# Kernel tuning notes

Hardware: AMD Instinct MI355X
Metric: run time of the kernel (lower is better)

Reference implementation:

```python
import jax, jax.numpy as jnp
import numpy as np

B, S, HID = 2, 2048, 4096
NH, NKV, HD = 32, 8, 128
SLIDING_WINDOW = 1024
ROPE_THETA = 10000.0


def setup_inputs() -> dict:
    key = jax.random.key(0)
    ks = jax.random.split(key, 6)
    hidden_states = jax.random.normal(ks[0], (B, S, HID), dtype=jnp.float32)
    attention_mask = jnp.ones((B, S), dtype=jnp.int32)
    position_ids = jnp.broadcast_to(jnp.arange(S, dtype=jnp.int32)[None, :], (B, S))
    sc = 1.0 / np.sqrt(HID)
    q_w = jax.random.normal(ks[1], (HID, NH * HD), dtype=jnp.float32) * sc
    k_w = jax.random.normal(ks[2], (HID, NKV * HD), dtype=jnp.float32) * sc
    v_w = jax.random.normal(ks[3], (HID, NKV * HD), dtype=jnp.float32) * sc
    o_w = jax.random.normal(ks[4], (NH * HD, HID), dtype=jnp.float32) * sc
    return {"hidden_states": hidden_states, "attention_mask": attention_mask,
            "position_ids": position_ids, "q_w": q_w, "k_w": k_w, "v_w": v_w, "o_w": o_w}


def _rotate_half(x):
    return jnp.concatenate((-x[..., x.shape[-1] // 2:], x[..., : x.shape[-1] // 2]), axis=-1)


def _rope_sincos(position_ids):
    # inv_freq over even dims of head_dim; emb = concat(freqs, freqs)
    inv_freq = 1.0 / ROPE_THETA ** (jnp.arange(0, HD, 2, dtype=jnp.float32) / HD)
    freqs = position_ids.astype(jnp.float32)[..., None] * inv_freq  # [B,S,HD/2]
    emb = jnp.concatenate((freqs, freqs), axis=-1)                  # [B,S,HD]
    # broadcast over heads axis: [B,S,1,HD]
    return jnp.sin(emb)[:, :, None, :], jnp.cos(emb)[:, :, None, :]


def reference(hidden_states, attention_mask, position_ids, q_w, k_w, v_w, o_w):
    b, q_len, _ = hidden_states.shape
    n_rep = NH // NKV

    q = (hidden_states @ q_w).reshape(b, q_len, NH, HD)
    k = (hidden_states @ k_w).reshape(b, q_len, NKV, HD)
    v = (hidden_states @ v_w).reshape(b, q_len, NKV, HD)

    sin_pos, cos_pos = _rope_sincos(position_ids)
    q = q * cos_pos + _rotate_half(q) * sin_pos
    k = k * cos_pos + _rotate_half(k) * sin_pos

    # GQA: repeat kv heads (repeat_interleave along head axis)
    k = jnp.repeat(k, n_rep, axis=2)  # [B,S,NH,HD]
    v = jnp.repeat(v, n_rep, axis=2)

    # sliding-window causal mask: j <= i and j >= i - sliding_window
    i = jnp.arange(q_len)[:, None]
    j = jnp.arange(q_len)[None, :]
    band = (j <= i) & (j >= i - SLIDING_WINDOW)           # [Q,K]
    mask = band[None, None] & (attention_mask[:, None, None, :] > 0)  # [B,1,Q,K]

    bias = jnp.where(mask, 0.0, jnp.finfo(jnp.float32).min)

    scale = 1.0 / jnp.sqrt(jnp.asarray(HD, dtype=jnp.float32))
    scores = jnp.einsum('bqhd,bkhd->bhqk', q, k) * scale + bias
    attn_weights = jax.nn.softmax(scores, axis=-1)
    attn_out = jnp.einsum('bhqk,bkhd->bqhd', attn_weights, v)
    attn_out = attn_out.reshape(b, q_len, HID)
    return attn_out @ o_w
```

## Files before the change

kernel.cpp:

```cpp
#include <hip/hip_runtime.h>
#include <stdint.h>
#include <stddef.h>

typedef __bf16 bf16x8 __attribute__((ext_vector_type(8)));
typedef short short8 __attribute__((ext_vector_type(8)));
typedef float floatx4 __attribute__((ext_vector_type(4)));
typedef float f32x16 __attribute__((ext_vector_type(16)));
typedef unsigned short ushort4v __attribute__((ext_vector_type(4)));
typedef unsigned int uint2v __attribute__((ext_vector_type(2)));

__device__ __forceinline__ unsigned short f2bf(float f){
  unsigned int u = __float_as_uint(f);
  u += 0x7fffu + ((u >> 16) & 1u);
  return (unsigned short)(u >> 16);
}
__device__ __forceinline__ float bf2f(unsigned short s){
  return __uint_as_float(((unsigned int)s) << 16);
}
__device__ __forceinline__ void gl2lds16(const void* g, void* l){
  __builtin_amdgcn_global_load_lds((const __attribute__((address_space(1))) void*)g,
                                   (__attribute__((address_space(3))) void*)l, 16, 0, 0);
}

__global__ __launch_bounds__(256) void conv_f32_bf16(const float* __restrict__ in,
                                                     unsigned short* __restrict__ out){
  int t = blockIdx.x * 256 + threadIdx.x;
  floatx4 v = *(const floatx4*)(in + (size_t)t * 4);
  ushort4v o;
#pragma unroll
  for (int j = 0; j < 4; ++j) o[j] = f2bf(v[j]);
  *(ushort4v*)(out + (size_t)t * 4) = o;
}

__global__ __launch_bounds__(256) void transpose_cvt(const float* __restrict__ in,
                                                     unsigned short* __restrict__ out,
                                                     int Kd, int Nd){
  __shared__ __align__(16) unsigned short tile[64 * 80];
  int n0 = blockIdx.x * 64, k0 = blockIdx.y * 64;
  int t = threadIdx.x;
#pragma unroll
  for (int it = 0; it < 2; ++it){
    int rr = (t >> 3) + it * 32;
    int cc = t & 7;
    const float* src = in + (size_t)(k0 + rr) * Nd + n0 + cc * 8;
    floatx4 a = *(const floatx4*)src;
    floatx4 b = *(const floatx4*)(src + 4);
    short8 s;
#pragma unroll
    for (int j = 0; j < 4; ++j){ s[j] = (short)f2bf(a[j]); s[j + 4] = (short)f2bf(b[j]); }
    *(short8*)&tile[rr * 80 + cc * 8] = s;
  }
  __syncthreads();
#pragma unroll
  for (int it = 0; it < 2; ++it){
    int nr = (t >> 3) + it * 32;
    int kc = t & 7;
    short8 v;
#pragma unroll
    for (int j = 0; j < 8; ++j) v[j] = (short)tile[(kc * 8 + j) * 80 + nr];
    *(short8*)(out + (size_t)(n0 + nr) * Kd + k0 + kc * 8) = v;
  }
}

__global__ __launch_bounds__(512, 2) void gemm_bt(
    const unsigned short* __restrict__ A,
    const unsigned short* __restrict__ Wq,
    const unsigned short* __restrict__ Wk,
    const unsigned short* __restrict__ Wv,
    unsigned short* __restrict__ oQ,
    unsigned short* __restrict__ oK,
    unsigned short* __restrict__ oVt,
    float* __restrict__ oF, int f32out)
{
  __shared__ __align__(16) unsigned short As[2][256 * 64];
  __shared__ __align__(16) unsigned short Bs[2][256 * 64];
  const int tid = threadIdx.x;
  const int w = tid >> 6, lane = tid & 63, quad = lane >> 4, l15 = lane & 15;
  const int wr = w >> 2, wc = w & 3;
  const int m0 = blockIdx.y * 256;
  const int n0 = blockIdx.x * 256;

  const unsigned short* Wsrc;
  int nb, region;
  if (n0 < 4096)      { Wsrc = Wq; nb = n0;        region = 0; }
  else if (n0 < 5120) { Wsrc = Wk; nb = n0 - 4096; region = 1; }
  else                { Wsrc = Wv; nb = n0 - 5120; region = 2; }

  floatx4 acc[8][4];
#pragma unroll
  for (int i = 0; i < 8; ++i)
#pragma unroll
    for (int j = 0; j < 4; ++j) acc[i][j] = (floatx4){0.f, 0.f, 0.f, 0.f};

#define STG(SRC, ROW0, H, DST, K0)                                                     \
  { _Pragma("unroll")                                                                  \
    for (int rep_ = 0; rep_ < 2; ++rep_){                                              \
      int u_ = tid + rep_ * 512;                                                       \
      int r_ = (H) * 128 + (u_ >> 3);                                                  \
      int c_ = u_ & 7;                                                                 \
      gl2lds16((SRC) + ((size_t)((ROW0) + r_) << 12) + (K0) + ((c_ ^ (r_ & 7)) << 3),  \
               (char*)(DST) + (H) * 16384 + (size_t)u_ * 16);                          \
    } }

  STG(A,    m0, 0, &As[0][0], 0);
  STG(Wsrc, nb, 0, &Bs[0][0], 0);
  STG(Wsrc, nb, 1, &Bs[0][0], 0);
  STG(A,    m0, 1, &As[0][0], 0);
  asm volatile("s_waitcnt vmcnt(4)" ::: "memory");
  __builtin_amdgcn_s_barrier();

  for (int t = 0; t < 64; ++t){
    const int cb = t & 1, nbuf = cb ^ 1;
    const int s = (t < 63) ? (t + 1) : 63;
    const int kn = s << 6;
    const unsigned short* Ac = &As[cb][0];
    const unsigned short* Bc = &Bs[cb][0];

    bf16x8 af[4][2], bf0[2][2], bf1[2][2];

#pragma unroll
    for (int i = 0; i < 4; ++i){
      int r = (wr * 4 + i) * 16 + l15;
#pragma unroll
      for (int ks = 0; ks < 2; ++ks){
        int kc = ks * 4 + quad;
        af[i][ks] = *(const bf16x8*)&Ac[r * 64 + ((kc ^ (r & 7)) << 3)];
      }
    }
#pragma unroll
    for (int j = 0; j < 2; ++j){
      int r = (wc * 2 + j) * 16 + l15;
#pragma unroll
      for (int ks = 0; ks < 2; ++ks){
        int kc = ks * 4 + quad;
        bf0[j][ks] = *(const bf16x8*)&Bc[r * 64 + ((kc ^ (r & 7)) << 3)];
      }
    }
    STG(A, m0, 0, &As[nbuf][0], kn);
    __builtin_amdgcn_s_setprio(1);
#pragma unroll
    for (int i = 0; i < 4; ++i)
#pragma unroll
      for (int j = 0; j < 2; ++j)
#pragma unroll
        for (int ks = 0; ks < 2; ++ks)
          acc[i][j] = __builtin_amdgcn_mfma_f32_16x16x32_bf16(af[i][ks], bf0[j][ks], acc[i][j], 0, 0, 0);
    __builtin_amdgcn_s_setprio(0);
    asm volatile("s_waitcnt vmcnt(4)" ::: "memory");
    __builtin_amdgcn_s_barrier();

#pragma unroll
    for (int j = 0; j < 2; ++j){
      int r = (8 + wc * 2 + j) * 16 + l15;
#pragma unroll
      for (int ks = 0; ks < 2; ++ks){
        int kc = ks * 4 + quad;
        bf1[j][ks] = *(const bf16x8*)&Bc[r * 64 + ((kc ^ (r & 7)) << 3)];
      }
    }
    STG(Wsrc, nb, 0, &Bs[nbuf][0], kn);
    __builtin_amdgcn_s_setprio(1);
#pragma unroll
    for (int i = 0; i < 4; ++i)
#pragma unroll
      for (int j = 0; j < 2; ++j)
#pragma unroll
        for (int ks = 0; ks < 2; ++ks)
          acc[i][2 + j] = __builtin_amdgcn_mfma_f32_16x16x32_bf16(af[i][ks], bf1[j][ks], acc[i][2 + j], 0, 0, 0);
    __builtin_amdgcn_s_setprio(0);
    asm volatile("s_waitcnt vmcnt(4)" ::: "memory");
    __builtin_amdgcn_s_barrier();

#pragma unroll
    for (int i = 0; i < 4; ++i){
      int r = (8 + wr * 4 + i) * 16 + l15;
#pragma unroll
      for (int ks = 0; ks < 2; ++ks){
        int kc = ks * 4 + quad;
        af[i][ks] = *(const bf16x8*)&Ac[r * 64 + ((kc ^ (r & 7)) << 3)];
      }
    }
    STG(Wsrc, nb, 1, &Bs[nbuf][0], kn);
    __builtin_amdgcn_s_setprio(1);
#pragma unroll
    for (int i = 0; i < 4; ++i)
#pragma unroll
      for (int j = 0; j < 2; ++j)
#pragma unroll
        for (int ks = 0; ks < 2; ++ks)
          acc[4 + i][2 + j] = __builtin_amdgcn_mfma_f32_16x16x32_bf16(af[i][ks], bf1[j][ks], acc[4 + i][2 + j], 0, 0, 0);
    __builtin_amdgcn_s_setprio(0);
    __builtin_amdgcn_s_barrier();

#pragma unroll
    for (int j = 0; j < 2; ++j){
      int r = (wc * 2 + j) * 16 + l15;
#pragma unroll
      for (int ks = 0; ks < 2; ++ks){
        int kc = ks * 4 + quad;
        bf0[j][ks] = *(const bf16x8*)&Bc[r * 64 + ((kc ^ (r & 7)) << 3)];
      }
    }
    STG(A, m0, 1, &As[nbuf][0], kn);
    __builtin_amdgcn_s_setprio(1);
#pragma unroll
    for (int i = 0; i < 4; ++i)
#pragma unroll
      for (int j = 0; j < 2; ++j)
#pragma unroll
        for (int ks = 0; ks < 2; ++ks)
          acc[4 + i][j] = __builtin_amdgcn_mfma_f32_16x16x32_bf16(af[i][ks], bf0[j][ks], acc[4 + i][j], 0, 0, 0);
    __builtin_amdgcn_s_setprio(0);
    asm volatile("s_waitcnt vmcnt(4)" ::: "memory");
    __builtin_amdgcn_s_barrier();
  }
#undef STG

  if (region == 0){
    if (f32out){
#pragma unroll
      for (int mi = 0; mi < 8; ++mi){
        const int row = (mi >> 2) * 128 + wr * 64 + (mi & 3) * 16 + quad * 4;
#pragma unroll
        for (int nj = 0; nj < 4; ++nj){
          const int gn = n0 + (nj >> 1) * 128 + wc * 32 + (nj & 1) * 16 + l15;
#pragma unroll
          for (int rr = 0; rr < 4; ++rr){
            const int gm = m0 + row + rr;
            oF[((size_t)gm << 12) + gn] = acc[mi][nj][rr];
          }
        }
      }
    } else {
#pragma unroll
      for (int mi = 0; mi < 8; ++mi){
        const int row = (mi >> 2) * 128 + wr * 64 + (mi & 3) * 16 + quad * 4;
#pragma unroll
        for (int nj = 0; nj < 4; ++nj){
          const int gn = n0 + (nj >> 1) * 128 + wc * 32 + (nj & 1) * 16 + l15;
#pragma unroll
          for (int rr = 0; rr < 4; ++rr){
            const int gm = m0 + row + rr;
            oQ[((size_t)gm << 12) + gn] = f2bf(acc[mi][nj][rr]);
          }
        }
      }
    }
  } else if (region == 1){
#pragma unroll
    for (int mi = 0; mi < 8; ++mi){
      const int row = (mi >> 2) * 128 + wr * 64 + (mi & 3) * 16 + quad * 4;
#pragma unroll
      for (int nj = 0; nj < 4; ++nj){
        const int gn = n0 - 4096 + (nj >> 1) * 128 + wc * 32 + (nj & 1) * 16 + l15;
#pragma unroll
        for (int rr = 0; rr < 4; ++rr){
          const int gm = m0 + row + rr;
          oK[((size_t)gm << 10) + gn] = f2bf(acc[mi][nj][rr]);
        }
      }
    }
  } else {
#pragma unroll
    for (int mi = 0; mi < 8; ++mi){
      const int gm0 = m0 + (mi >> 2) * 128 + wr * 64 + (mi & 3) * 16 + quad * 4;
      const int b = gm0 >> 11, s0 = gm0 & 2047;
#pragma unroll
      for (int nj = 0; nj < 4; ++nj){
        const int dg = n0 - 5120 + (nj >> 1) * 128 + wc * 32 + (nj & 1) * 16 + l15;
        const int kvh = dg >> 7, d = dg & 127;
        ushort4v pk;
#pragma unroll
        for (int rr = 0; rr < 4; ++rr) pk[rr] = f2bf(acc[mi][nj][rr]);
        *(ushort4v*)(oVt + (((size_t)(b * 8 + kvh) * 128 + d) * 2048 + s0)) = pk;
      }
    }
  }
}

__global__ void rope_apply_k(unsigned short* __restrict__ Qb, unsigned short* __restrict__ Kb,
                             const int* __restrict__ pos){
  int t = blockIdx.x * 256 + threadIdx.x;
  unsigned short* base;
  int row, ch;
  bool isq = (t < 1048576);
  if (isq){ row = t >> 8; int c = t & 255; base = Qb + ((size_t)row << 12) + (c >> 3) * 128; ch = c & 7; }
  else { int t2 = t - 1048576; row = t2 >> 6; int c = t2 & 63; base = Kb + ((size_t)row << 10) + (c >> 3) * 128; ch = c & 7; }
  float p = (float)pos[row];
  const float qs = 0.08838834764831845f * 1.44269504088896340736f;
  float sc_out = isq ? qs : 1.0f;
  int d0 = ch * 8;
  short8 x0 = *(short8*)(base + d0);
  short8 x1 = *(short8*)(base + d0 + 64);
  short8 y0, y1;
#pragma unroll
  for (int j = 0; j < 8; ++j){
    float ang = p * exp2f(-(float)(d0 + j) * 0.20762050593045952f);
    float sn = sinf(ang), cs = cosf(ang);
    float a  = bf2f((unsigned short)x0[j]);
    float bb = bf2f((unsigned short)x1[j]);
    y0[j] = (short)f2bf((a * cs - bb * sn) * sc_out);
    y1[j] = (short)f2bf((bb * cs + a * sn) * sc_out);
  }
  *(short8*)(base + d0)      = y0;
  *(short8*)(base + d0 + 64) = y1;
}

__global__ __launch_bounds__(256, 2) void flash_swa(
    const unsigned short* __restrict__ Q,
    const unsigned short* __restrict__ K,
    const unsigned short* __restrict__ Vt,
    const int* __restrict__ amask,
    unsigned short* __restrict__ attn)
{
  __shared__ __align__(16) unsigned short Kl[2][64 * 128];
  __shared__ __align__(16) unsigned short Vl[2][128 * 64];
  __shared__ __align__(16) unsigned int   Pl[4][1024];
  const int h = blockIdx.y, b = blockIdx.z;
  const int kv = h >> 2;
  const int tid = threadIdx.x, w = tid >> 6, lane = tid & 63;
  const int l31 = lane & 31, hi = lane >> 5, hi4 = hi << 2;
  const int qb = blockIdx.x * 128;
  const int t0 = qb >> 6;
  const int qw0 = qb + w * 32;
  const int aw = t0 + (w >> 1);

  bool anybad = false;
  {
    const int* ap = amask + b * 2048 + lane * 32;
#pragma unroll
    for (int i = 0; i < 8; ++i){
      int4 mv = *(const int4*)(ap + i * 4);
      anybad |= (mv.x <= 0) | (mv.y <= 0) | (mv.z <= 0) | (mv.w <= 0);
    }
  }
  const bool allv = (__ballot(anybad) == 0ull);

  bf16x8 qf[8];
  {
    const unsigned short* qbase = Q + (((size_t)(b * 2048 + qw0 + l31)) << 12) + h * 128;
#pragma unroll
    for (int ds = 0; ds < 8; ++ds) qf[ds] = *(const bf16x8*)(qbase + ds * 16 + hi * 8);
  }

  f32x16 acco[4];
#pragma unroll
  for (int i = 0; i < 4; ++i)
#pragma unroll
    for (int j = 0; j < 16; ++j) acco[i][j] = 0.f;
  float m_i = -1e30f, l_i = 0.f;

  const int jb0 = (t0 >= 16) ? (t0 - 16) : 0;
  const int jtend = t0 + 1;

#define STAGE_KV(JT, BUF)                                                                  \
  {                                                                                        \
    const int k0s = (JT) * 64;                                                             \
    _Pragma("unroll")                                                                      \
    for (int i_ = 0; i_ < 4; ++i_){                                                        \
      int u_ = i_ * 4 + w;                                                                 \
      int r_ = u_ * 4 + (lane >> 4);                                                       \
      int c_ = lane & 15;                                                                  \
      gl2lds16(K + (((size_t)(b * 2048 + k0s + r_)) << 10) + kv * 128 + ((c_ ^ (r_ & 15)) << 3), \
               (char*)Kl[BUF] + u_ * 1024);                                                \
    }                                                                                      \
    _Pragma("unroll")                                                                      \
    for (int i_ = 0; i_ < 4; ++i_){                                                        \
      int u_ = i_ * 4 + w;                                                                 \
      int d_ = u_ * 8 + (lane >> 3);                                                       \
      int c_ = lane & 7;                                                                   \
      gl2lds16(Vt + ((size_t)(b * 8 + kv) * 128 + d_) * 2048 + k0s + ((c_ ^ (d_ & 7)) << 3), \
               (char*)Vl[BUF] + u_ * 1024);                                                \
    }                                                                                      \
  }

  STAGE_KV(jb0, 0);
  __syncthreads();

  unsigned int* Pw = &Pl[w][0];
  int cur = 0;
  for (int jt = jb0; jt <= jtend; ++jt){
    if (jt < jtend) STAGE_KV(jt + 1, cur ^ 1);

    const bool active = (jt >= aw - 16) && (jt <= aw);
    if (active){
      const int k0 = jt * 64;
      const unsigned short* Klc = Kl[cur];
      const unsigned short* Vlc = Vl[cur];

      f32x16 ps[2];
#pragma unroll
      for (int kb = 0; kb < 2; ++kb)
#pragma unroll
        for (int j = 0; j < 16; ++j) ps[kb][j] = 0.f;

      __builtin_amdgcn_s_setprio(1);
#pragma unroll
      for (int ds = 0; ds < 8; ++ds){
#pragma unroll
        for (int kb = 0; kb < 2; ++kb){
          int r = kb * 32 + l31;
          bf16x8 kf = *(const bf16x8*)&Klc[r * 128 + (((ds * 2 + hi) ^ (r & 15)) << 3)];
          ps[kb] = __builtin_amdgcn_mfma_f32_32x32x16_bf16(kf, qf[ds], ps[kb], 0, 0, 0);
        }
      }
      __builtin_amdgcn_s_setprio(0);

      const bool slow = (jt == aw) || (jt == aw - 16) || (!allv);
      if (slow){
        unsigned long long mb = __ballot(amask[b * 2048 + k0 + lane] > 0);
        int irow = qw0 + l31;
#pragma unroll
        for (int kb = 0; kb < 2; ++kb)
#pragma unroll
          for (int reg = 0; reg < 16; ++reg){
            int jv = k0 + kb * 32 + (reg & 3) + 8 * (reg >> 2) + hi4;
            bool valid = (jv <= irow) && (jv >= irow - 1024) &&
                         (((mb >> (jv & 63)) & 1ull) != 0ull);
            ps[kb][reg] = valid ? ps[kb][reg] : -1e30f;
          }
      }

      float t16[16];
#pragma unroll
      for (int r = 0; r < 16; ++r) t16[r] = fmaxf(ps[0][r], ps[1][r]);
      float t8[8];
#pragma unroll
      for (int r = 0; r < 8; ++r) t8[r] = fmaxf(t16[r], t16[r + 8]);
      float t4[4];
#pragma unroll
      for (int r = 0; r < 4; ++r) t4[r] = fmaxf(t8[r], t8[r + 4]);
      float vm = fmaxf(fmaxf(t4[0], t4[1]), fmaxf(t4[2], t4[3]));
      float vmax = fmaxf(vm, __shfl_xor(vm, 32));

      if (!__all(vmax - m_i <= 8.0f)){
        float mnew = fmaxf(m_i, vmax);
        float alpha = exp2f(m_i - mnew);
        m_i = mnew;
        l_i *= alpha;
#pragma unroll
        for (int db = 0; db < 4; ++db) acco[db] *= alpha;
      }

#pragma unroll
      for (int kb = 0; kb < 2; ++kb)
#pragma unroll
        for (int reg = 0; reg < 16; ++reg) ps[kb][reg] = exp2f(ps[kb][reg] - m_i);

      float s16[16];
#pragma unroll
      for (int r = 0; r < 16; ++r) s16[r] = ps[0][r] + ps[1][r];
      float s8[8];
#pragma unroll
      for (int r = 0; r < 8; ++r) s8[r] = s16[r] + s16[r + 8];
      float s4[4];
#pragma unroll
      for (int r = 0; r < 4; ++r) s4[r] = s8[r] + s8[r + 4];
      float sm = (s4[0] + s4[1]) + (s4[2] + s4[3]);
      l_i += sm + __shfl_xor(sm, 32);

#pragma unroll
      for (int kb = 0; kb < 2; ++kb)
#pragma unroll
        for (int g = 0; g < 4; ++g){
          unsigned p0 = (unsigned)f2bf(ps[kb][g * 4 + 0]) | ((unsigned)f2bf(ps[kb][g * 4 + 1]) << 16);
          unsigned p1 = (unsigned)f2bf(ps[kb][g * 4 + 2]) | ((unsigned)f2bf(ps[kb][g * 4 + 3]) << 16);
          int ch = (kb * 4 + g) ^ (l31 & 7);
          uint2v pv_; pv_[0] = p0; pv_[1] = p1;
          *(uint2v*)&Pw[l31 * 32 + ch * 4 + hi * 2] = pv_;
        }
      bf16x8 pa[4];
#pragma unroll
      for (int ks = 0; ks < 4; ++ks)
        pa[ks] = *(const bf16x8*)&Pw[l31 * 32 + (((ks * 2 + hi) ^ (l31 & 7)) << 2)];

      __builtin_amdgcn_s_setprio(1);
#pragma unroll
      for (int ks = 0; ks < 4; ++ks){
#pragma unroll
        for (int db = 0; db < 4; ++db){
          int d = db * 32 + l31;
          bf16x8 vf = *(const bf16x8*)&Vlc[d * 64 + (((ks * 2 + hi) ^ (d & 7)) << 3)];
          acco[db] = __builtin_amdgcn_mfma_f32_32x32x16_bf16(vf, pa[ks], acco[db], 0, 0, 0);
        }
      }
      __builtin_amdgcn_s_setprio(0);
    }

    __syncthreads();
    cur ^= 1;
  }
#undef STAGE_KV

  float invl = 1.f / l_i;
  unsigned short* Ep = ((unsigned short*)Kl) + w * 4096;
  {
    const int q = l31;
#pragma unroll
    for (int db = 0; db < 4; ++db)
#pragma unroll
      for (int reg = 0; reg < 16; ++reg){
        int dc = db * 4 + (reg >> 2);
        int dl = (reg & 3) + hi4;
        Ep[q * 128 + ((dc ^ (q & 15)) << 3) + dl] = f2bf(acco[db][reg] * invl);
      }
  }
  {
    const int rr_ = lane >> 4, cc = lane & 15;
#pragma unroll
    for (int p8 = 0; p8 < 8; ++p8){
      int q = p8 * 4 + rr_;
      short8 vv = *(const short8*)&Ep[q * 128 + ((cc ^ (q & 15)) << 3)];
      size_t off = (((size_t)(b * 2048 + qb + w * 32 + q)) << 12) + h * 128 + cc * 8;
      *(short8*)(attn + off) = vv;
    }
  }
}

extern "C" void kernel_launch(void* const* d_in, const int* in_sizes, int n_in,
                              void* d_out, int out_size, void* d_ws, size_t ws_size,
                              hipStream_t stream){
  const float* hidden = (const float*)d_in[0];
  const int* amask = (const int*)d_in[1];
  const int* pos   = (const int*)d_in[2];
  const float* qw = (const float*)d_in[3];
  const float* kw = (const float*)d_in[4];
  const float* vw = (const float*)d_in[5];
  const float* ow = (const float*)d_in[6];

  char* ws = (char*)d_ws;
  unsigned short* hb   = (unsigned short*)(ws + 0);
  unsigned short* qt   = (unsigned short*)(ws + 33554432);
  unsigned short* kt   = (unsigned short*)(ws + 67108864);
  unsigned short* vtw  = (unsigned short*)(ws + 75497472);
  unsigned short* Qb   = (unsigned short*)(ws + 83886080);
  unsigned short* Kb   = (unsigned short*)(ws + 117440512);
  unsigned short* Vtb  = (unsigned short*)(ws + 125829120);
  unsigned short* ot   = hb;
  unsigned short* attn = qt;
  float* outp = (float*)d_out;

  hipLaunchKernelGGL(conv_f32_bf16, dim3(16384), dim3(256), 0, stream, hidden, hb);
  hipLaunchKernelGGL(transpose_cvt, dim3(64, 64), dim3(256), 0, stream, qw, qt, 4096, 4096);
  hipLaunchKernelGGL(transpose_cvt, dim3(16, 64), dim3(256), 0, stream, kw, kt, 4096, 1024);
  hipLaunchKernelGGL(transpose_cvt, dim3(16, 64), dim3(256), 0, stream, vw, vtw, 4096, 1024);
  hipLaunchKernelGGL(gemm_bt, dim3(24, 16), dim3(512), 0, stream,
                     hb, qt, kt, vtw, Qb, Kb, Vtb, (float*)nullptr, 0);
  hipLaunchKernelGGL(transpose_cvt, dim3(64, 64), dim3(256), 0, stream, ow, ot, 4096, 4096);
  hipLaunchKernelGGL(rope_apply_k, dim3(5120), dim3(256), 0, stream, Qb, Kb, pos);
  hipLaunchKernelGGL(flash_swa, dim3(16, 32, 2), dim3(256), 0, stream, Qb, Kb, Vtb, amask, attn);
  hipLaunchKernelGGL(gemm_bt, dim3(16, 16), dim3(512), 0, stream,
                     attn, ot, ot, ot, nullptr, nullptr, nullptr, outp, 1);
}
```

Before: 699.8 us.

## Fuse prep conversions into one launch and use 128x128 tiles for QKV GEMM

Merges the hidden-state conversion and the three weight transpose-convert kernels into one launch that dispatches on block index, removing three launches. It also replaces the 256x256 double-buffered QKV projection GEMM with a new 128x128, 256-thread kernel that uses a single LDS buffer. The grid grows from 384 to 1536 blocks, which should fill the CUs better, but the new kernel has no load/compute overlap and less data reuse per tile.

Result: no change. 707.7 us (+1.1%).

```diff
diff --git a/kernel.cpp b/kernel.cpp
--- a/kernel.cpp
+++ b/kernel.cpp
@@ -22,22 +22,11 @@
                                    (__attribute__((address_space(3))) void*)l, 16, 0, 0);
 }
 
-__global__ __launch_bounds__(256) void conv_f32_bf16(const float* __restrict__ in,
-                                                     unsigned short* __restrict__ out){
-  int t = blockIdx.x * 256 + threadIdx.x;
-  floatx4 v = *(const floatx4*)(in + (size_t)t * 4);
-  ushort4v o;
-#pragma unroll
-  for (int j = 0; j < 4; ++j) o[j] = f2bf(v[j]);
-  *(ushort4v*)(out + (size_t)t * 4) = o;
-}
-
-__global__ __launch_bounds__(256) void transpose_cvt(const float* __restrict__ in,
-                                                     unsigned short* __restrict__ out,
-                                                     int Kd, int Nd){
-  __shared__ __align__(16) unsigned short tile[64 * 80];
-  int n0 = blockIdx.x * 64, k0 = blockIdx.y * 64;
-  int t = threadIdx.x;
+__device__ __forceinline__ void transpose_body(const float* __restrict__ in,
+                                               unsigned short* __restrict__ out,
+                                               int Kd, int Nd, int bx, int by, int t,
+                                               unsigned short* tile){
+  int n0 = bx * 64, k0 = by * 64;
 #pragma unroll
   for (int it = 0; it < 2; ++it){
     int rr = (t >> 3) + it * 32;
@@ -62,7 +51,164 @@
   }
 }
 
-__global__ __launch_bounds__(512, 2) void gemm_bt(
+__global__ __launch_bounds__(256) void transpose_cvt(const float* __restrict__ in,
+                                                     unsigned short* __restrict__ out,
+                                                     int Kd, int Nd){
+  __shared__ __align__(16) unsigned short tile[64 * 80];
+  transpose_body(in, out, Kd, Nd, blockIdx.x, blockIdx.y, threadIdx.x, tile);
+}
+
+__global__ __launch_bounds__(256) void prep_fused(const float* __restrict__ hidden,
+                                                  unsigned short* __restrict__ hb,
+                                                  const float* __restrict__ qw,
+                                                  unsigned short* __restrict__ qtw,
+                                                  const float* __restrict__ kw,
+                                                  unsigned short* __restrict__ kt,
+                                                  const float* __restrict__ vw,
+                                                  unsigned short* __restrict__ vtw){
+  __shared__ __align__(16) unsigned short tile[64 * 80];
+  const int bid = blockIdx.x, t = threadIdx.x;
+  if (bid < 16384){
+    int i = bid * 256 + t;
+    floatx4 v = *(const floatx4*)(hidden + (size_t)i * 4);
+    ushort4v o;
+#pragma unroll
+    for (int j = 0; j < 4; ++j) o[j] = f2bf(v[j]);
+    *(ushort4v*)(hb + (size_t)i * 4) = o;
+  } else if (bid < 20480){
+    int b2 = bid - 16384;
+    transpose_body(qw, qtw, 4096, 4096, b2 & 63, b2 >> 6, t, tile);
+  } else if (bid < 21504){
+    int b2 = bid - 20480;
+    transpose_body(kw, kt, 4096, 1024, b2 & 15, b2 >> 4, t, tile);
+  } else {
+    int b2 = bid - 21504;
+    transpose_body(vw, vtw, 4096, 1024, b2 & 15, b2 >> 4, t, tile);
+  }
+}
+
+__global__ __launch_bounds__(256, 2) void gemm_bt128(
+    const unsigned short* __restrict__ A,
+    const unsigned short* __restrict__ Wq,
+    const unsigned short* __restrict__ Wk,
+    const unsigned short* __restrict__ Wv,
+    unsigned short* __restrict__ oQ,
+    unsigned short* __restrict__ oK,
+    unsigned short* __restrict__ oVt,
+    float* __restrict__ oF, int f32out)
+{
+  __shared__ __align__(16) unsigned short As[128 * 64];
+  __shared__ __align__(16) unsigned short Bs[128 * 64];
+  const int tid = threadIdx.x;
+  const int w = tid >> 6, lane = tid & 63, quad = lane >> 4, l15 = lane & 15;
+  const int wm64 = (w >> 1) * 64, wn64 = (w & 1) * 64;
+  const int m0 = blockIdx.y * 128;
+  const int n0 = blockIdx.x * 128;
+
+  const unsigned short* Wsrc;
+  int nb, region;
+  if (n0 < 4096)      { Wsrc = Wq; nb = n0;        region = 0; }
+  else if (n0 < 5120) { Wsrc = Wk; nb = n0 - 4096; region = 1; }
+  else                { Wsrc = Wv; nb = n0 - 5120; region = 2; }
+
+  floatx4 acc[4][4];
+#pragma unroll
+  for (int i = 0; i < 4; ++i)
+#pragma unroll
+    for (int j = 0; j < 4; ++j) acc[i][j] = (floatx4){0.f, 0.f, 0.f, 0.f};
+
+  const int rsub = lane >> 3, csub = lane & 7;
+
+  for (int k0 = 0; k0 < 4096; k0 += 64){
+#pragma unroll
+    for (int i = 0; i < 4; ++i){
+      int u = i * 4 + w;
+      int r = u * 8 + rsub;
+      gl2lds16(A    + ((size_t)(m0 + r) << 12) + k0 + ((csub ^ (r & 7)) << 3), (char*)As + u * 1024);
+      gl2lds16(Wsrc + ((size_t)(nb + r) << 12) + k0 + ((csub ^ (r & 7)) << 3), (char*)Bs + u * 1024);
+    }
+    __syncthreads();
+#pragma unroll
+    for (int ks = 0; ks < 2; ++ks){
+      bf16x8 af[4], bfr[4];
+#pragma unroll
+      for (int mt = 0; mt < 4; ++mt){
+        int r = wm64 + mt * 16 + l15;
+        int kc = ks * 4 + quad;
+        af[mt] = *(const bf16x8*)&As[r * 64 + ((kc ^ (r & 7)) << 3)];
+      }
+#pragma unroll
+      for (int nt = 0; nt < 4; ++nt){
+        int r = wn64 + nt * 16 + l15;
+        int kc = ks * 4 + quad;
+        bfr[nt] = *(const bf16x8*)&Bs[r * 64 + ((kc ^ (r & 7)) << 3)];
+      }
+#pragma unroll
+      for (int mt = 0; mt < 4; ++mt)
+#pragma unroll
+        for (int nt = 0; nt < 4; ++nt)
+          acc[mt][nt] = __builtin_amdgcn_mfma_f32_16x16x32_bf16(af[mt], bfr[nt], acc[mt][nt], 0, 0, 0);
+    }
+    __syncthreads();
+  }
+
+  if (region == 0){
+    if (f32out){
+#pragma unroll
+      for (int mt = 0; mt < 4; ++mt)
+#pragma unroll
+        for (int nt = 0; nt < 4; ++nt){
+          int gn = n0 + wn64 + nt * 16 + l15;
+#pragma unroll
+          for (int rr = 0; rr < 4; ++rr){
+            int gm = m0 + wm64 + mt * 16 + quad * 4 + rr;
+            oF[((size_t)gm << 12) + gn] = acc[mt][nt][rr];
+          }
+        }
+    } else {
+#pragma unroll
+      for (int mt = 0; mt < 4; ++mt)
+#pragma unroll
+        for (int nt = 0; nt < 4; ++nt){
+          int gn = n0 + wn64 + nt * 16 + l15;
+#pragma unroll
+          for (int rr = 0; rr < 4; ++rr){
+            int gm = m0 + wm64 + mt * 16 + quad * 4 + rr;
+            oQ[((size_t)gm << 12) + gn] = f2bf(acc[mt][nt][rr]);
+          }
+        }
+    }
+  } else if (region == 1){
+#pragma unroll
+    for (int mt = 0; mt < 4; ++mt)
+#pragma unroll
+      for (int nt = 0; nt < 4; ++nt){
+        int gn = n0 - 4096 + wn64 + nt * 16 + l15;
+#pragma unroll
+        for (int rr = 0; rr < 4; ++rr){
+          int gm = m0 + wm64 + mt * 16 + quad * 4 + rr;
+          oK[((size_t)gm << 10) + gn] = f2bf(acc[mt][nt][rr]);
+        }
+      }
+  } else {
+#pragma unroll
+    for (int mt = 0; mt < 4; ++mt){
+      int gm0 = m0 + wm64 + mt * 16 + quad * 4;
+      int b = gm0 >> 11, s0 = gm0 & 2047;
+#pragma unroll
+      for (int nt = 0; nt < 4; ++nt){
+        int dg = n0 - 5120 + wn64 + nt * 16 + l15;
+        int kvh = dg >> 7, d = dg & 127;
+        ushort4v pk;
+#pragma unroll
+        for (int rr = 0; rr < 4; ++rr) pk[rr] = f2bf(acc[mt][nt][rr]);
+        *(ushort4v*)(oVt + (((size_t)(b * 8 + kvh) * 128 + d) * 2048 + s0)) = pk;
+      }
+    }
+  }
+}
+
+__global__ __launch_bounds__(512, 2) void gemm_bt256(
     const unsigned short* __restrict__ A,
     const unsigned short* __restrict__ Wq,
     const unsigned short* __restrict__ Wk,
@@ -540,15 +686,13 @@
   unsigned short* attn = qt;
   float* outp = (float*)d_out;
 
-  hipLaunchKernelGGL(conv_f32_bf16, dim3(16384), dim3(256), 0, stream, hidden, hb);
-  hipLaunchKernelGGL(transpose_cvt, dim3(64, 64), dim3(256), 0, stream, qw, qt, 4096, 4096);
-  hipLaunchKernelGGL(transpose_cvt, dim3(16, 64), dim3(256), 0, stream, kw, kt, 4096, 1024);
-  hipLaunchKernelGGL(transpose_cvt, dim3(16, 64), dim3(256), 0, stream, vw, vtw, 4096, 1024);
-  hipLaunchKernelGGL(gemm_bt, dim3(24, 16), dim3(512), 0, stream,
+  hipLaunchKernelGGL(prep_fused, dim3(22528), dim3(256), 0, stream,
+                     hidden, hb, qw, qt, kw, kt, vw, vtw);
+  hipLaunchKernelGGL(gemm_bt128, dim3(48, 32), dim3(256), 0, stream,
                      hb, qt, kt, vtw, Qb, Kb, Vtb, (float*)nullptr, 0);
   hipLaunchKernelGGL(transpose_cvt, dim3(64, 64), dim3(256), 0, stream, ow, ot, 4096, 4096);
   hipLaunchKernelGGL(rope_apply_k, dim3(5120), dim3(256), 0, stream, Qb, Kb, pos);
   hipLaunchKernelGGL(flash_swa, dim3(16, 32, 2), dim3(256), 0, stream, Qb, Kb, Vtb, amask, attn);
-  hipLaunchKernelGGL(gemm_bt, dim3(16, 16), dim3(512), 0, stream,
+  hipLaunchKernelGGL(gemm_bt256, dim3(16, 16), dim3(512), 0, stream,
                      attn, ot, ot, ot, nullptr, nullptr, nullptr, outp, 1);
 }
```
